# Kernel optimization log

Measured on AMD Instinct MI355X. Metric: run time of the kernel, lower is better.

The kernel has to match this reference:

```python
import jax, jax.numpy as jnp
import numpy as np

WS = 7          # window size
SHIFT = 3       # shift size (window_size // 2)
RES = 56        # input resolution
DIMS = 192      # channel dim
HEADS = DIMS // 32
HD = DIMS // HEADS
N = WS * WS     # tokens per window (49)
NW = (RES // WS) ** 2  # windows per image (64)


def _position_index():
    # matches tf.meshgrid(coords_w, coords_h)[::-1] stacking
    coords = np.stack(np.meshgrid(np.arange(WS), np.arange(WS))[::-1])  # (2, ws, ws)
    flat = coords.reshape(2, -1)                                        # (2, N)
    rel = (flat[:, :, None] - flat[:, None, :]).transpose(1, 2, 0)      # (N, N, 2)
    h = (rel[..., 0] + WS - 1) * (2 * WS - 1)
    w = rel[..., 1] + WS - 1
    return (h + w).reshape(-1)                                          # (N*N,)


def _swin_mask():
    img = np.zeros((RES, RES))
    cnt = 0
    sls = (slice(0, -WS), slice(-WS, -SHIFT), slice(-SHIFT, None))
    for hs in sls:
        for ws_ in sls:
            img[hs, ws_] = cnt
            cnt += 1
    # window partition
    m = img.reshape(RES // WS, WS, RES // WS, WS).transpose(0, 2, 1, 3).reshape(-1, N)
    a = m[:, None, :] - m[:, :, None]            # (nW, N, N)
    a = np.where(a == 0, 0.0, -1000.0).astype(np.float32)
    return a[:, None]                            # (nW, 1, N, N)


_PIDX = _position_index()
_MASK = _swin_mask()


def setup_inputs() -> dict:
    key = jax.random.key(0)
    ks = jax.random.split(key, 6)
    s = 0.02
    return {
        "x": jax.random.normal(ks[0], (64, RES, RES, DIMS), jnp.float32),
        "table": jax.random.normal(ks[1], ((2 * WS - 1) ** 2, HEADS), jnp.float32) * s,
        "wq": jax.random.normal(ks[2], (DIMS, DIMS), jnp.float32) * s,
        "bq": jnp.zeros((DIMS,), jnp.float32),
        "wk": jax.random.normal(ks[3], (DIMS, DIMS), jnp.float32) * s,
        "bk": jnp.zeros((DIMS,), jnp.float32),
        "wv": jax.random.normal(ks[4], (DIMS, DIMS), jnp.float32) * s,
        "bv": jnp.zeros((DIMS,), jnp.float32),
        "wo": jax.random.normal(ks[5], (DIMS, DIMS), jnp.float32) * s,
        "bo": jnp.zeros((DIMS,), jnp.float32),
    }


def reference(x, table, wq, bq, wk, bk, wv, bv, wo, bo):
    B = x.shape[0]
    # gathered relative-position bias: (1, heads, N, N)
    bias = table[_PIDX].reshape(N, N, HEADS).transpose(2, 0, 1)[None]
    mask = jnp.asarray(_MASK)  # (nW, 1, N, N)

    # cyclic shift + window partition
    xs = jnp.roll(x, (-SHIFT, -SHIFT), axis=(1, 2))
    xw = xs.reshape(B, RES // WS, WS, RES // WS, WS, DIMS)
    xw = xw.transpose(0, 1, 3, 2, 4, 5).reshape(-1, N, DIMS)  # (B*nW, N, C)
    BW = xw.shape[0]

    def split_heads(t):
        return t.reshape(BW, N, HEADS, HD).transpose(0, 2, 1, 3)  # (BW, h, N, hd)

    q = split_heads(xw @ wq + bq)
    k = split_heads(xw @ wk + bk)
    v = split_heads(xw @ wv + bv)

    scores = jnp.einsum('bhqd,bhkd->bhqk', q, k) / jnp.sqrt(jnp.float32(HD))
    scores = scores + bias
    # matches tf.repeat(mask, B // W, axis=0) in the original code
    scores = scores + jnp.repeat(mask, BW // NW, axis=0)
    attn = jax.nn.softmax(scores, axis=-1)
    o = jnp.einsum('bhqk,bhkd->bhqd', attn, v)
    o = o.transpose(0, 2, 1, 3).reshape(BW, N, DIMS)
    o = o @ wo + bo

    # window reverse + reverse cyclic shift
    o = o.reshape(B, RES // WS, RES // WS, WS, WS, DIMS)
    o = o.transpose(0, 1, 3, 2, 4, 5).reshape(B, RES, RES, DIMS)
    return jnp.roll(o, (SHIFT, SHIFT), axis=(1, 2))
```

## Files before the change

kernel.cpp:

```cpp
#include <hip/hip_runtime.h>


typedef __attribute__((ext_vector_type(8))) short bf16x8;
typedef __attribute__((ext_vector_type(4))) short short4v;
typedef __attribute__((ext_vector_type(4))) float f32x4;

__device__ __forceinline__ short f2bf(float x) {
  unsigned u = __builtin_bit_cast(unsigned, x);
  u += 0x7fffu + ((u >> 16) & 1u);
  return (short)(u >> 16);
}

__device__ __forceinline__ unsigned cvtpk(float a, float b) {
  unsigned r;
  asm("v_cvt_pk_bf16_f32 %0, %1, %2" : "=v"(r) : "v"(a), "v"(b));
  return r;
}

__global__ void prep_kernel(const float* __restrict__ wq, const float* __restrict__ wk,
                            const float* __restrict__ wv, const float* __restrict__ wo,
                            const float* __restrict__ table,
                            short* __restrict__ wT, float* __restrict__ biasx) {
  int tid = blockIdx.x * 256 + threadIdx.x;
  if (tid < 4 * 36864) {
    int mat = tid / 36864, rem = tid % 36864;
    int k = rem / 192, n = rem % 192;
    const float* w = (mat == 0) ? wq : (mat == 1) ? wk : (mat == 2) ? wv : wo;
    wT[mat * 36864 + n * 192 + k] = f2bf(w[k * 192 + n]);
  }
  if (tid < 6 * 2548) {
    int h = tid / 2548, rem = tid % 2548;
    int q = rem / 52, k = rem % 52;
    float v = 0.f;
    if (k < 49) {
      int idx = ((q / 7) - (k / 7) + 6) * 13 + ((q % 7) - (k % 7) + 6);
      v = table[idx * 6 + h];
    }
    biasx[h * 2548 + q * 52 + k] = v;
  }
}

__launch_bounds__(768, 3)
__global__ void swin_attn_kernel(const float* __restrict__ x,
                                 const short* __restrict__ wT,
                                 const float* __restrict__ biasx,
                                 const float* __restrict__ bq, const float* __restrict__ bk,
                                 const float* __restrict__ bv, const float* __restrict__ bo,
                                 float* __restrict__ out) {
  extern __shared__ short smem[];
  short* s_xo = smem;
  short* s_q  = smem + 12800;
  short* s_k  = smem + 25600;
  short* s_vt = smem + 38400;
  short* s_p  = smem + 52224;

  const int tid  = threadIdx.x;
  const int w    = tid >> 6;
  const int lane = tid & 63;
  const int quad = lane >> 4;
  const int l15  = lane & 15;

  const int bw  = blockIdx.x;
  const int b   = bw >> 6;
  const int wi  = bw & 63;
  const int wwh = wi >> 3, www = wi & 7;
  const int mwh = b >> 3,  mww = b & 7;

  const int rt = w & 3;
  const int g  = w >> 2;

  const f32x4 zero4 = {0.f, 0.f, 0.f, 0.f};
  const float NEGINF = -__builtin_inff();
  const float SCALE = 0.17677669529663687f;

  {
    const int hb = wwh * 7 + 3, wb = www * 7 + 3;
    for (int i = tid; i < 2352; i += 768) {
      int t = i / 48, c4 = i - t * 48;
      int th = t / 7, tw = t - th * 7;
      int gh = hb + th; if (gh >= 56) gh -= 56;
      int gw = wb + tw; if (gw >= 56) gw -= 56;
      float4 v = *(const float4*)(x + (((b * 56 + gh) * 56 + gw) * 192 + c4 * 4));
      uint2 s;
      s.x = cvtpk(v.x, v.y); s.y = cvtpk(v.z, v.w);
      *(uint2*)(s_xo + t * 200 + c4 * 4) = s;
    }
  }
  __syncthreads();

  {
    bf16x8 xf[4][6];
#pragma unroll
    for (int nt = 0; nt < 4; ++nt)
#pragma unroll
      for (int ks = 0; ks < 6; ++ks)
        xf[nt][ks] = *(const bf16x8*)(s_xo + (nt * 16 + l15) * 200 + ks * 32 + quad * 8);

    const short* wtm = wT + g * 36864;
    if (g < 2) {
      const float* bp = g ? bk : bq;
      short* dst = g ? s_k : s_q;
#pragma unroll
      for (int i = 0; i < 3; ++i) {
        const int dbase = (rt * 3 + i) * 16;
        const short* wrow = wtm + (dbase + l15) * 192;
        bf16x8 wf[6];
#pragma unroll
        for (int ks = 0; ks < 6; ++ks)
          wf[ks] = *(const bf16x8*)(wrow + ks * 32 + quad * 8);
        f32x4 acc[4] = {zero4, zero4, zero4, zero4};
        __builtin_amdgcn_s_setprio(1);
#pragma unroll
        for (int ks = 0; ks < 6; ++ks)
#pragma unroll
          for (int nt = 0; nt < 4; ++nt)
            acc[nt] = __builtin_amdgcn_mfma_f32_16x16x32_bf16(wf[ks], xf[nt][ks], acc[nt], 0, 0, 0);
        __builtin_amdgcn_s_setprio(0);
        const float4 b4 = *(const float4*)(bp + dbase + quad * 4);
#pragma unroll
        for (int nt = 0; nt < 4; ++nt) {
          const int tok = nt * 16 + l15;
          const bool tv = (tok < 49);
          float e0 = tv ? acc[nt][0] + b4.x : 0.f;
          float e1 = tv ? acc[nt][1] + b4.y : 0.f;
          float e2 = tv ? acc[nt][2] + b4.z : 0.f;
          float e3 = tv ? acc[nt][3] + b4.w : 0.f;
          uint2 st;
          st.x = cvtpk(e0, e1); st.y = cvtpk(e2, e3);
          *(uint2*)(dst + tok * 200 + dbase + quad * 4) = st;
        }
      }
    } else {
#pragma unroll
      for (int i = 0; i < 3; ++i) {
        const int dbase = (rt * 3 + i) * 16;
        const short* wrow = wtm + (dbase + l15) * 192;
        bf16x8 wf[6];
#pragma unroll
        for (int ks = 0; ks < 6; ++ks)
          wf[ks] = *(const bf16x8*)(wrow + ks * 32 + quad * 8);
        f32x4 acc[4] = {zero4, zero4, zero4, zero4};
        __builtin_amdgcn_s_setprio(1);
#pragma unroll
        for (int ks = 0; ks < 6; ++ks)
#pragma unroll
          for (int nt = 0; nt < 4; ++nt)
            acc[nt] = __builtin_amdgcn_mfma_f32_16x16x32_bf16(xf[nt][ks], wf[ks], acc[nt], 0, 0, 0);
        __builtin_amdgcn_s_setprio(0);
        const float bvv = bv[dbase + l15];
#pragma unroll
        for (int nt = 0; nt < 4; ++nt) {
          float e[4];
#pragma unroll
          for (int r = 0; r < 4; ++r) {
            int key = nt * 16 + quad * 4 + r;
            e[r] = (key < 49) ? (acc[nt][r] + bvv) : 0.f;
          }
          uint2 st;
          st.x = cvtpk(e[0], e[1]); st.y = cvtpk(e[2], e[3]);
          *(uint2*)(s_vt + (dbase + l15) * 72 + nt * 16 + quad * 4) = st;
        }
      }
    }
  }
  __syncthreads();

  const int token = rt * 16 + l15;
  const int qc  = (token < 49) ? token : 48;
  {
    const int qth = qc / 7, qtw = qc - qth * 7;
    const int cq  = ((mwh == 7) ? (1 + (qth >= 4)) : 0) * 3
                  + ((mww == 7) ? (1 + (qtw >= 4)) : 0);
    float bmadd[4][4];
#pragma unroll
    for (int mt = 0; mt < 4; ++mt) {
#pragma unroll
      for (int r = 0; r < 4; ++r) {
        int key = mt * 16 + quad * 4 + r;
        if (key > 48) {
          bmadd[mt][r] = NEGINF;
        } else {
          int kth = key / 7, ktw = key - kth * 7;
          int ck = ((mwh == 7) ? (1 + (kth >= 4)) : 0) * 3
                 + ((mww == 7) ? (1 + (ktw >= 4)) : 0);
          bmadd[mt][r] = (ck == cq) ? 0.f : -1000.f;
        }
      }
    }

    short* myp = s_p + w * 1152;
#pragma unroll
    for (int hh = 0; hh < 2; ++hh) {
      const int h = g * 2 + hh;
      const int d0 = h * 32;
      const float* bxr = biasx + h * 2548 + qc * 52;
      f32x4 b4[4];
#pragma unroll
      for (int mt = 0; mt < 4; ++mt) {
        const int kc = (mt < 3) ? (mt * 16 + quad * 4) : 48;
        b4[mt] = *(const f32x4*)(bxr + kc);
      }
      bf16x8 qf = *(const bf16x8*)(s_q + (rt * 16 + l15) * 200 + d0 + quad * 8);
      float sv[4][4];
#pragma unroll
      for (int mt = 0; mt < 4; ++mt) {
        bf16x8 kf = *(const bf16x8*)(s_k + (mt * 16 + l15) * 200 + d0 + quad * 8);
        f32x4 s = __builtin_amdgcn_mfma_f32_16x16x32_bf16(kf, qf, zero4, 0, 0, 0);
#pragma unroll
        for (int r = 0; r < 4; ++r)
          sv[mt][r] = s[r] * SCALE + b4[mt][r] + bmadd[mt][r];
      }
      float mx = sv[0][0];
#pragma unroll
      for (int mt = 0; mt < 4; ++mt)
#pragma unroll
        for (int r = 0; r < 4; ++r) mx = fmaxf(mx, sv[mt][r]);
      mx = fmaxf(mx, __shfl_xor(mx, 16));
      mx = fmaxf(mx, __shfl_xor(mx, 32));
      float s0 = 0.f;
#pragma unroll
      for (int mt = 0; mt < 4; ++mt)
#pragma unroll
        for (int r = 0; r < 4; ++r) {
          float e = __expf(sv[mt][r] - mx);
          sv[mt][r] = e;
          s0 += e;
        }
      s0 += __shfl_xor(s0, 16);
      s0 += __shfl_xor(s0, 32);
      const float inv = 1.0f / s0;
#pragma unroll
      for (int mt = 0; mt < 4; ++mt) {
        uint2 st;
        st.x = cvtpk(sv[mt][0], sv[mt][1]); st.y = cvtpk(sv[mt][2], sv[mt][3]);
        *(uint2*)(myp + l15 * 72 + mt * 16 + quad * 4) = st;
      }
#pragma unroll
      for (int mt2 = 0; mt2 < 2; ++mt2) {
        f32x4 o = zero4;
#pragma unroll
        for (int ks = 0; ks < 2; ++ks) {
          bf16x8 vfr = *(const bf16x8*)(s_vt + (d0 + mt2 * 16 + l15) * 72 + ks * 32 + quad * 8);
          bf16x8 pfr = *(const bf16x8*)(myp + l15 * 72 + ks * 32 + quad * 8);
          o = __builtin_amdgcn_mfma_f32_16x16x32_bf16(vfr, pfr, o, 0, 0, 0);
        }
        uint2 st;
        st.x = cvtpk(o[0] * inv, o[1] * inv); st.y = cvtpk(o[2] * inv, o[3] * inv);
        *(uint2*)(s_xo + (rt * 16 + l15) * 200 + d0 + mt2 * 16 + quad * 4) = st;
      }
    }
  }

  const int cbase = w * 16;
  const short* wrow4 = wT + 3 * 36864 + (cbase + l15) * 192;
  bf16x8 wf4[6];
#pragma unroll
  for (int ks = 0; ks < 6; ++ks)
    wf4[ks] = *(const bf16x8*)(wrow4 + ks * 32 + quad * 8);

  __syncthreads();

  {
    bf16x8 ao[4][6];
#pragma unroll
    for (int nt = 0; nt < 4; ++nt)
#pragma unroll
      for (int ks = 0; ks < 6; ++ks)
        ao[nt][ks] = *(const bf16x8*)(s_xo + (nt * 16 + l15) * 200 + ks * 32 + quad * 8);

    f32x4 acc[4] = {zero4, zero4, zero4, zero4};
    __builtin_amdgcn_s_setprio(1);
#pragma unroll
    for (int ks = 0; ks < 6; ++ks)
#pragma unroll
      for (int nt = 0; nt < 4; ++nt)
        acc[nt] = __builtin_amdgcn_mfma_f32_16x16x32_bf16(wf4[ks], ao[nt][ks], acc[nt], 0, 0, 0);
    __builtin_amdgcn_s_setprio(0);

    const float4 bo4 = *(const float4*)(bo + cbase + quad * 4);
#pragma unroll
    for (int nt = 0; nt < 4; ++nt) {
      const int tok = nt * 16 + l15;
      if (tok < 49) {
        int tth = tok / 7, ttw = tok - tth * 7;
        int gh = wwh * 7 + tth + 3; if (gh >= 56) gh -= 56;
        int gw = www * 7 + ttw + 3; if (gw >= 56) gw -= 56;
        float4 v;
        v.x = acc[nt][0] + bo4.x; v.y = acc[nt][1] + bo4.y;
        v.z = acc[nt][2] + bo4.z; v.w = acc[nt][3] + bo4.w;
        *(float4*)(out + ((b * 56 + gh) * 56 + gw) * 192 + cbase + quad * 4) = v;
      }
    }
  }
}

extern "C" void kernel_launch(void* const* d_in, const int* in_sizes, int n_in,
                              void* d_out, int out_size, void* d_ws, size_t ws_size,
                              hipStream_t stream) {
  const float* x     = (const float*)d_in[0];
  const float* table = (const float*)d_in[1];
  const float* wq    = (const float*)d_in[2];
  const float* bq    = (const float*)d_in[3];
  const float* wk    = (const float*)d_in[4];
  const float* bk    = (const float*)d_in[5];
  const float* wv    = (const float*)d_in[6];
  const float* bv    = (const float*)d_in[7];
  const float* wo    = (const float*)d_in[8];
  const float* bo    = (const float*)d_in[9];
  float* out = (float*)d_out;

  short* wT    = (short*)d_ws;
  float* biasx = (float*)((char*)d_ws + 294912);

  prep_kernel<<<576, 256, 0, stream>>>(wq, wk, wv, wo, table, wT, biasx);

  const int smem_bytes = 66048 * 2;
  (void)hipFuncSetAttribute(reinterpret_cast<const void*>(swin_attn_kernel),
                            hipFuncAttributeMaxDynamicSharedMemorySize, smem_bytes);
  swin_attn_kernel<<<4096, 768, smem_bytes, stream>>>(x, wT, biasx, bq, bk, bv, bo, out);
}
```

Measured before the change: 480.4 us.

## Prefetch QKV weights before barrier and interleave two heads' attention

Moves the global loads of the QKV weight fragments ahead of the first barrier so they overlap the x staging. The relative-position bias is now loaded before the barrier that guards the attention phase. The two heads' score MFMAs and softmaxes are interleaved, each with its own P buffer, so independent work can hide latency. The cost is more registers (18 weight fragments held live) and more LDS (about 156 KB per block), which may cut occupancy or add spills.

```diff
diff --git a/kernel.cpp b/kernel.cpp
--- a/kernel.cpp
+++ b/kernel.cpp
@@ -86,6 +86,18 @@
       *(uint2*)(s_xo + t * 200 + c4 * 4) = s;
     }
   }
+
+  bf16x8 wfp[3][6];
+  {
+    const short* wtm = wT + g * 36864;
+#pragma unroll
+    for (int i = 0; i < 3; ++i) {
+      const short* wrow = wtm + ((rt * 3 + i) * 16 + l15) * 192;
+#pragma unroll
+      for (int ks = 0; ks < 6; ++ks)
+        wfp[i][ks] = *(const bf16x8*)(wrow + ks * 32 + quad * 8);
+    }
+  }
   __syncthreads();
 
   {
@@ -96,25 +108,19 @@
       for (int ks = 0; ks < 6; ++ks)
         xf[nt][ks] = *(const bf16x8*)(s_xo + (nt * 16 + l15) * 200 + ks * 32 + quad * 8);
 
-    const short* wtm = wT + g * 36864;
     if (g < 2) {
       const float* bp = g ? bk : bq;
       short* dst = g ? s_k : s_q;
 #pragma unroll
       for (int i = 0; i < 3; ++i) {
         const int dbase = (rt * 3 + i) * 16;
-        const short* wrow = wtm + (dbase + l15) * 192;
-        bf16x8 wf[6];
-#pragma unroll
-        for (int ks = 0; ks < 6; ++ks)
-          wf[ks] = *(const bf16x8*)(wrow + ks * 32 + quad * 8);
         f32x4 acc[4] = {zero4, zero4, zero4, zero4};
         __builtin_amdgcn_s_setprio(1);
 #pragma unroll
         for (int ks = 0; ks < 6; ++ks)
 #pragma unroll
           for (int nt = 0; nt < 4; ++nt)
-            acc[nt] = __builtin_amdgcn_mfma_f32_16x16x32_bf16(wf[ks], xf[nt][ks], acc[nt], 0, 0, 0);
+            acc[nt] = __builtin_amdgcn_mfma_f32_16x16x32_bf16(wfp[i][ks], xf[nt][ks], acc[nt], 0, 0, 0);
         __builtin_amdgcn_s_setprio(0);
         const float4 b4 = *(const float4*)(bp + dbase + quad * 4);
 #pragma unroll
@@ -134,18 +140,13 @@
 #pragma unroll
       for (int i = 0; i < 3; ++i) {
         const int dbase = (rt * 3 + i) * 16;
-        const short* wrow = wtm + (dbase + l15) * 192;
-        bf16x8 wf[6];
-#pragma unroll
-        for (int ks = 0; ks < 6; ++ks)
-          wf[ks] = *(const bf16x8*)(wrow + ks * 32 + quad * 8);
         f32x4 acc[4] = {zero4, zero4, zero4, zero4};
         __builtin_amdgcn_s_setprio(1);
 #pragma unroll
         for (int ks = 0; ks < 6; ++ks)
 #pragma unroll
           for (int nt = 0; nt < 4; ++nt)
-            acc[nt] = __builtin_amdgcn_mfma_f32_16x16x32_bf16(xf[nt][ks], wf[ks], acc[nt], 0, 0, 0);
+            acc[nt] = __builtin_amdgcn_mfma_f32_16x16x32_bf16(xf[nt][ks], wfp[i][ks], acc[nt], 0, 0, 0);
         __builtin_amdgcn_s_setprio(0);
         const float bvv = bv[dbase + l15];
 #pragma unroll
@@ -163,15 +164,14 @@
       }
     }
   }
-  __syncthreads();
 
   const int token = rt * 16 + l15;
   const int qc  = (token < 49) ? token : 48;
+  float bmadd[4][4];
   {
     const int qth = qc / 7, qtw = qc - qth * 7;
     const int cq  = ((mwh == 7) ? (1 + (qth >= 4)) : 0) * 3
                   + ((mww == 7) ? (1 + (qtw >= 4)) : 0);
-    float bmadd[4][4];
 #pragma unroll
     for (int mt = 0; mt < 4; ++mt) {
 #pragma unroll
@@ -187,34 +187,49 @@
         }
       }
     }
-
-    short* myp = s_p + w * 1152;
-#pragma unroll
-    for (int hh = 0; hh < 2; ++hh) {
-      const int h = g * 2 + hh;
-      const int d0 = h * 32;
-      const float* bxr = biasx + h * 2548 + qc * 52;
-      f32x4 b4[4];
+  }
+  f32x4 b4h[2][4];
+#pragma unroll
+  for (int hh = 0; hh < 2; ++hh) {
+    const float* bxr = biasx + (g * 2 + hh) * 2548 + qc * 52;
+#pragma unroll
+    for (int mt = 0; mt < 4; ++mt) {
+      const int kc = (mt < 3) ? (mt * 16 + quad * 4) : 48;
+      b4h[hh][mt] = *(const f32x4*)(bxr + kc);
+    }
+  }
+  __syncthreads();
+
+  {
+    short* myp0 = s_p + w * 2304;
+    short* myp1 = myp0 + 1152;
+    const int d00 = g * 64, d01 = g * 64 + 32;
+    const int qrow = (rt * 16 + l15) * 200;
+
+    float sv0[4][4], sv1[4][4];
+    {
+      bf16x8 qf0 = *(const bf16x8*)(s_q + qrow + d00 + quad * 8);
+      bf16x8 qf1 = *(const bf16x8*)(s_q + qrow + d01 + quad * 8);
 #pragma unroll
       for (int mt = 0; mt < 4; ++mt) {
-        const int kc = (mt < 3) ? (mt * 16 + quad * 4) : 48;
-        b4[mt] = *(const f32x4*)(bxr + kc);
-      }
-      bf16x8 qf = *(const bf16x8*)(s_q + (rt * 16 + l15) * 200 + d0 + quad * 8);
-      float sv[4][4];
-#pragma unroll
-      for (int mt = 0; mt < 4; ++mt) {
-        bf16x8 kf = *(const bf16x8*)(s_k + (mt * 16 + l15) * 200 + d0 + quad * 8);
-        f32x4 s = __builtin_amdgcn_mfma_f32_16x16x32_bf16(kf, qf, zero4, 0, 0, 0);
-#pragma unroll
-        for (int r = 0; r < 4; ++r)
-          sv[mt][r] = s[r] * SCALE + b4[mt][r] + bmadd[mt][r];
-      }
-      float mx = sv[0][0];
+        bf16x8 kf0 = *(const bf16x8*)(s_k + (mt * 16 + l15) * 200 + d00 + quad * 8);
+        bf16x8 kf1 = *(const bf16x8*)(s_k + (mt * 16 + l15) * 200 + d01 + quad * 8);
+        f32x4 s0 = __builtin_amdgcn_mfma_f32_16x16x32_bf16(kf0, qf0, zero4, 0, 0, 0);
+        f32x4 s1 = __builtin_amdgcn_mfma_f32_16x16x32_bf16(kf1, qf1, zero4, 0, 0, 0);
+#pragma unroll
+        for (int r = 0; r < 4; ++r) {
+          sv0[mt][r] = s0[r] * SCALE + b4h[0][mt][r] + bmadd[mt][r];
+          sv1[mt][r] = s1[r] * SCALE + b4h[1][mt][r] + bmadd[mt][r];
+        }
+      }
+    }
+    float inv0;
+    {
+      float mx = sv0[0][0];
 #pragma unroll
       for (int mt = 0; mt < 4; ++mt)
 #pragma unroll
-        for (int r = 0; r < 4; ++r) mx = fmaxf(mx, sv[mt][r]);
+        for (int r = 0; r < 4; ++r) mx = fmaxf(mx, sv0[mt][r]);
       mx = fmaxf(mx, __shfl_xor(mx, 16));
       mx = fmaxf(mx, __shfl_xor(mx, 32));
       float s0 = 0.f;
@@ -222,32 +237,73 @@
       for (int mt = 0; mt < 4; ++mt)
 #pragma unroll
         for (int r = 0; r < 4; ++r) {
-          float e = __expf(sv[mt][r] - mx);
-          sv[mt][r] = e;
+          float e = __expf(sv0[mt][r] - mx);
+          sv0[mt][r] = e;
           s0 += e;
         }
       s0 += __shfl_xor(s0, 16);
       s0 += __shfl_xor(s0, 32);
-      const float inv = 1.0f / s0;
+      inv0 = 1.0f / s0;
 #pragma unroll
       for (int mt = 0; mt < 4; ++mt) {
         uint2 st;
-        st.x = cvtpk(sv[mt][0], sv[mt][1]); st.y = cvtpk(sv[mt][2], sv[mt][3]);
-        *(uint2*)(myp + l15 * 72 + mt * 16 + quad * 4) = st;
-      }
-#pragma unroll
-      for (int mt2 = 0; mt2 < 2; ++mt2) {
-        f32x4 o = zero4;
-#pragma unroll
-        for (int ks = 0; ks < 2; ++ks) {
-          bf16x8 vfr = *(const bf16x8*)(s_vt + (d0 + mt2 * 16 + l15) * 72 + ks * 32 + quad * 8);
-          bf16x8 pfr = *(const bf16x8*)(myp + l15 * 72 + ks * 32 + quad * 8);
-          o = __builtin_amdgcn_mfma_f32_16x16x32_bf16(vfr, pfr, o, 0, 0, 0);
-        }
+        st.x = cvtpk(sv0[mt][0], sv0[mt][1]); st.y = cvtpk(sv0[mt][2], sv0[mt][3]);
+        *(uint2*)(myp0 + l15 * 72 + mt * 16 + quad * 4) = st;
+      }
+    }
+    float inv1;
+    {
+      float mx = sv1[0][0];
+#pragma unroll
+      for (int mt = 0; mt < 4; ++mt)
+#pragma unroll
+        for (int r = 0; r < 4; ++r) mx = fmaxf(mx, sv1[mt][r]);
+      mx = fmaxf(mx, __shfl_xor(mx, 16));
+      mx = fmaxf(mx, __shfl_xor(mx, 32));
+      float s0 = 0.f;
+#pragma unroll
+      for (int mt = 0; mt < 4; ++mt)
+#pragma unroll
+        for (int r = 0; r < 4; ++r) {
+          float e = __expf(sv1[mt][r] - mx);
+          sv1[mt][r] = e;
+          s0 += e;
+        }
+      s0 += __shfl_xor(s0, 16);
+      s0 += __shfl_xor(s0, 32);
+      inv1 = 1.0f / s0;
+#pragma unroll
+      for (int mt = 0; mt < 4; ++mt) {
         uint2 st;
-        st.x = cvtpk(o[0] * inv, o[1] * inv); st.y = cvtpk(o[2] * inv, o[3] * inv);
-        *(uint2*)(s_xo + (rt * 16 + l15) * 200 + d0 + mt2 * 16 + quad * 4) = st;
-      }
+        st.x = cvtpk(sv1[mt][0], sv1[mt][1]); st.y = cvtpk(sv1[mt][2], sv1[mt][3]);
+        *(uint2*)(myp1 + l15 * 72 + mt * 16 + quad * 4) = st;
+      }
+    }
+#pragma unroll
+    for (int mt2 = 0; mt2 < 2; ++mt2) {
+      f32x4 o = zero4;
+#pragma unroll
+      for (int ks = 0; ks < 2; ++ks) {
+        bf16x8 vfr = *(const bf16x8*)(s_vt + (d00 + mt2 * 16 + l15) * 72 + ks * 32 + quad * 8);
+        bf16x8 pfr = *(const bf16x8*)(myp0 + l15 * 72 + ks * 32 + quad * 8);
+        o = __builtin_amdgcn_mfma_f32_16x16x32_bf16(vfr, pfr, o, 0, 0, 0);
+      }
+      uint2 st;
+      st.x = cvtpk(o[0] * inv0, o[1] * inv0); st.y = cvtpk(o[2] * inv0, o[3] * inv0);
+      *(uint2*)(s_xo + qrow + d00 + mt2 * 16 + quad * 4) = st;
+    }
+#pragma unroll
+    for (int mt2 = 0; mt2 < 2; ++mt2) {
+      f32x4 o = zero4;
+#pragma unroll
+      for (int ks = 0; ks < 2; ++ks) {
+        bf16x8 vfr = *(const bf16x8*)(s_vt + (d01 + mt2 * 16 + l15) * 72 + ks * 32 + quad * 8);
+        bf16x8 pfr = *(const bf16x8*)(myp1 + l15 * 72 + ks * 32 + quad * 8);
+        o = __builtin_amdgcn_mfma_f32_16x16x32_bf16(vfr, pfr, o, 0, 0, 0);
+      }
+      uint2 st;
+      st.x = cvtpk(o[0] * inv1, o[1] * inv1); st.y = cvtpk(o[2] * inv1, o[3] * inv1);
+      *(uint2*)(s_xo + qrow + d01 + mt2 * 16 + quad * 4) = st;
     }
   }
 
@@ -314,7 +370,7 @@
 
   prep_kernel<<<576, 256, 0, stream>>>(wq, wk, wv, wo, table, wT, biasx);
 
-  const int smem_bytes = 66048 * 2;
+  const int smem_bytes = 79872 * 2;
   (void)hipFuncSetAttribute(reinterpret_cast<const void*>(swin_attn_kernel),
                             hipFuncAttributeMaxDynamicSharedMemorySize, smem_bytes);
   swin_attn_kernel<<<4096, 768, smem_bytes, stream>>>(x, wT, biasx, bq, bk, bv, bo, out);
```

New measurement: 545.6 us. 1.14x slower.
